# Optimization experiments

Hardware: AMD Instinct MI355X
Metric: run time of the kernel (lower is better)

Reference implementation:

```python
import jax, jax.numpy as jnp
import numpy as np

B, S, C = 4, 2048, 1024
E, H = 1024, 16
D = E // H  # head_dim = 64


def setup_inputs() -> dict:
    key = jax.random.key(0)
    k1, k2, k3, k4, k5 = jax.random.split(key, 5)
    s = 1.0 / np.sqrt(C)
    return {
        "x": jax.random.normal(k1, (B, S, C), dtype=jnp.float32),
        "w_qkv": jax.random.uniform(k2, (C, 3 * E), minval=-s, maxval=s, dtype=jnp.float32),
        "b_qkv": jax.random.uniform(k3, (3 * E,), minval=-s, maxval=s, dtype=jnp.float32),
        "w_out": jax.random.uniform(k4, (E, E), minval=-1.0 / np.sqrt(E), maxval=1.0 / np.sqrt(E), dtype=jnp.float32),
        "b_out": jax.random.uniform(k5, (E,), minval=-1.0 / np.sqrt(E), maxval=1.0 / np.sqrt(E), dtype=jnp.float32),
    }


def reference(x, w_qkv, b_qkv, w_out, b_out):
    b, s, _ = x.shape
    qkv = x @ w_qkv + b_qkv                      # [B,S,3E]
    qkv = qkv.reshape(b, s, 3, H, D)
    q = qkv[:, :, 0].transpose(0, 2, 1, 3)       # [B,H,S,D]
    k = qkv[:, :, 1].transpose(0, 2, 1, 3)
    v = qkv[:, :, 2].transpose(0, 2, 1, 3)
    scale = jnp.asarray(D, x.dtype) ** 0.5
    scores = jnp.einsum("bhqd,bhkd->bhqk", q, k) / scale
    attn = jax.nn.softmax(scores, axis=-1)       # dropout is identity in eval mode
    out = jnp.einsum("bhqk,bhkd->bhqd", attn, v)
    out = out.transpose(0, 2, 1, 3).reshape(b, s, E)
    return out @ w_out + b_out
```

## Files before the change

### kernel.cpp

```cpp
#include <hip/hip_runtime.h>


typedef _Float16 f16;
typedef f16 f16x2 __attribute__((ext_vector_type(2)));
typedef f16 f16x4 __attribute__((ext_vector_type(4)));
typedef f16 f16x8 __attribute__((ext_vector_type(8)));
typedef float f32x4 __attribute__((ext_vector_type(4)));

typedef const __attribute__((address_space(1))) void* gas_ptr;
typedef __attribute__((address_space(3))) void* lds_ptr;

__device__ __forceinline__ void load_lds16(const void* g, void* s) {
  __builtin_amdgcn_global_load_lds((gas_ptr)g, (lds_ptr)s, 16, 0, 0);
}

__device__ __forceinline__ f32x4 mfma16(f16x8 a, f16x8 b, f32x4 c) {
  return __builtin_amdgcn_mfma_f32_16x16x32_f16(a, b, c, 0, 0, 0);
}

__device__ __forceinline__ f16x2 pk2(float a, float b) {
  return __builtin_bit_cast(f16x2, __builtin_amdgcn_cvt_pkrtz(a, b));
}

__global__ __launch_bounds__(256) void cvt_x(const float* __restrict__ in, f16* __restrict__ out) {
  int i = blockIdx.x * 256 + threadIdx.x;
  const float4* p = (const float4*)in;
  float4 a = p[2 * i], b = p[2 * i + 1];
  f16x8 o;
  o[0] = (f16)a.x; o[1] = (f16)a.y; o[2] = (f16)a.z; o[3] = (f16)a.w;
  o[4] = (f16)b.x; o[5] = (f16)b.y; o[6] = (f16)b.z; o[7] = (f16)b.w;
  *(f16x8*)(out + 8 * (long)i) = o;
}

__global__ __launch_bounds__(256) void tconv(const float* __restrict__ in, f16* __restrict__ out,
                                             int R, int C) {
  __shared__ float t[32][33];
  int c0 = blockIdx.x * 32, r0 = blockIdx.y * 32;
  int tx = threadIdx.x, ty = threadIdx.y;
#pragma unroll
  for (int j = 0; j < 4; ++j)
    t[ty + 8 * j][tx] = in[(long)(r0 + ty + 8 * j) * C + c0 + tx];
  __syncthreads();
#pragma unroll
  for (int j = 0; j < 4; ++j)
    out[(long)(c0 + ty + 8 * j) * R + r0 + tx] = (f16)t[tx][ty + 8 * j];
}

__global__ __launch_bounds__(256) void qkv_gemm(const f16* __restrict__ A, const f16* __restrict__ BT,
                                                const float* __restrict__ bias,
                                                f16* __restrict__ Qs, f16* __restrict__ Kk,
                                                f16* __restrict__ Vt) {
  __shared__ __align__(16) f16 lA[2][128 * 64];
  __shared__ __align__(16) f16 lB[2][128 * 64];
  const int K = 1024;
  int tid = threadIdx.x, w = tid >> 6, lane = tid & 63, l16 = lane & 15, quad = lane >> 4;
  int wm = (w >> 1) * 64, wn = (w & 1) * 64;
  int id = blockIdx.y * gridDim.x + blockIdx.x;
  int xcd = id & 7, cch = id >> 3;
  int bx = xcd * 8 + (cch & 7), by = cch >> 3;
  int blockM = bx * 128, blockN = by * 128;
  int sw = l16 & 7;
  f32x4 acc[4][4] = {};

  auto stage = [&](int kt) {
    int k0 = kt * 64;
    f16* dA = lA[kt & 1];
    f16* dB = lB[kt & 1];
#pragma unroll
    for (int i = 0; i < 4; ++i) {
      int c = i * 256 + tid;
      int row = c >> 3;
      int sc = (c & 7) ^ (row & 7);
      load_lds16(A + (long)(blockM + row) * K + k0 + sc * 8, dA + c * 8);
      load_lds16(BT + (long)(blockN + row) * K + k0 + sc * 8, dB + c * 8);
    }
  };

  stage(0);
  asm volatile("s_waitcnt vmcnt(0)" ::: "memory");
  __builtin_amdgcn_s_barrier();

  for (int t = 0; t < 16; ++t) {
    if (t < 15) stage(t + 1);
    const f16* cA = lA[t & 1];
    const f16* cB = lB[t & 1];
#pragma unroll
    for (int ks = 0; ks < 2; ++ks) {
      f16x8 af[4], bf[4];
#pragma unroll
      for (int mb = 0; mb < 4; ++mb)
        af[mb] = *(const f16x8*)&cA[(wm + mb * 16 + l16) * 64 + ((ks * 4 + quad) ^ sw) * 8];
#pragma unroll
      for (int nb = 0; nb < 4; ++nb)
        bf[nb] = *(const f16x8*)&cB[(wn + nb * 16 + l16) * 64 + ((ks * 4 + quad) ^ sw) * 8];
      __builtin_amdgcn_s_setprio(1);
#pragma unroll
      for (int mb = 0; mb < 4; ++mb)
#pragma unroll
        for (int nb = 0; nb < 4; ++nb)
          acc[mb][nb] = mfma16(af[mb], bf[nb], acc[mb][nb]);
      __builtin_amdgcn_s_setprio(0);
    }
    asm volatile("s_waitcnt vmcnt(0)" ::: "memory");
    __builtin_amdgcn_s_barrier();
  }

  int which = by >> 3;
  const float SCALE = 0.18033688011112042f;
#pragma unroll
  for (int nb = 0; nb < 4; ++nb) {
    int col = blockN + wn + nb * 16 + l16;
    int hd = col & 1023, h = hd >> 6, d = hd & 63;
    float bv = bias[col];
#pragma unroll
    for (int mb = 0; mb < 4; ++mb) {
      int row0 = blockM + wm + mb * 16 + quad * 4;
      int b = row0 >> 11, s0 = row0 & 2047;
      if (which == 2) {
        f16x2 a = pk2(acc[mb][nb][0] + bv, acc[mb][nb][1] + bv);
        f16x2 c = pk2(acc[mb][nb][2] + bv, acc[mb][nb][3] + bv);
        *(f16x4*)&Vt[((b * 16 + h) * 64 + d) * 2048 + s0] =
            __builtin_shufflevector(a, c, 0, 1, 2, 3);
      } else if (which == 0) {
#pragma unroll
        for (int r = 0; r < 4; ++r)
          Qs[((b * 16 + h) * 2048 + s0 + r) * 64 + d] = (f16)((acc[mb][nb][r] + bv) * SCALE);
      } else {
#pragma unroll
        for (int r = 0; r < 4; ++r)
          Kk[((b * 16 + h) * 2048 + s0 + r) * 64 + d] = (f16)(acc[mb][nb][r] + bv);
      }
    }
  }
}

__global__ __launch_bounds__(512, 4) void attn(const f16* __restrict__ Qs, const f16* __restrict__ Kk,
                                               const f16* __restrict__ Vt, f16* __restrict__ ctx) {
  __shared__ __align__(16) f16 lK[2][64 * 72];
  __shared__ __align__(16) f16 lV[2][64 * 72];
  int id = blockIdx.y * gridDim.x + blockIdx.x;
  int swz = (id & 7) * 64 + (id >> 3);
  int qt = swz & 7, bh = swz >> 3;
  int tid = threadIdx.x, lane = tid & 63, l16 = lane & 15, quad = lane >> 4;
  int w = tid >> 6;
  const f16* Qbase = Qs + ((long)bh * 2048 + qt * 256 + w * 32) * 64;
  const f16* Kbh = Kk + (long)bh * 2048 * 64;
  const f16* Vbh = Vt + (long)bh * 64 * 2048;

  f16x8 qf[2][2];
#pragma unroll
  for (int rb = 0; rb < 2; ++rb)
#pragma unroll
    for (int ks = 0; ks < 2; ++ks)
      qf[rb][ks] = *(const f16x8*)(Qbase + (rb * 16 + l16) * 64 + ks * 32 + quad * 8);

  f32x4 of[2][4] = {};
  f32x4 osum[2] = {};
  const f16 one = (f16)1.f;
  const f16x8 vone8 = {one, one, one, one, one, one, one, one};

  int rs = tid >> 3, o = (tid & 7) * 8;
  int koff = o & 31;
  int cperm = (o & 32) + ((koff & 12) << 1) + ((koff >> 4) << 2);

  {
    *(float4*)&lK[0][rs * 72 + o] = *(const float4*)(Kbh + rs * 64 + o);
    float4 pv = *(const float4*)(Vbh + (long)rs * 2048 + o);
    f16x8 v8 = __builtin_bit_cast(f16x8, pv);
    *(f16x4*)&lV[0][rs * 72 + cperm] = __builtin_shufflevector(v8, v8, 0, 1, 2, 3);
    *(f16x4*)&lV[0][rs * 72 + cperm + 8] = __builtin_shufflevector(v8, v8, 4, 5, 6, 7);
  }
  __syncthreads();

  for (int kt = 0; kt < 32; ++kt) {
    int cur = kt & 1, nxt = cur ^ 1;

    float4 pk0, pv0;
    if (kt < 31) {
      int kb0 = (kt + 1) * 64;
      pk0 = *(const float4*)(Kbh + (kb0 + rs) * 64 + o);
      pv0 = *(const float4*)(Vbh + (long)rs * 2048 + kb0 + o);
    }

    __builtin_amdgcn_s_setprio(1);
#pragma unroll
    for (int kp = 0; kp < 2; ++kp) {
      f16x4 pah[2][2];
#pragma unroll
      for (int kbh = 0; kbh < 2; ++kbh) {
        int kb = kp * 2 + kbh;
        f16x8 kf0 = *(const f16x8*)&lK[cur][(kb * 16 + l16) * 72 + quad * 8];
        f16x8 kf1 = *(const f16x8*)&lK[cur][(kb * 16 + l16) * 72 + 32 + quad * 8];
#pragma unroll
        for (int rb = 0; rb < 2; ++rb) {
          f32x4 z = {};
          z = mfma16(kf0, qf[rb][0], z);
          z = mfma16(kf1, qf[rb][1], z);
          float p0 = __builtin_amdgcn_exp2f(z[0]);
          float p1 = __builtin_amdgcn_exp2f(z[1]);
          float p2 = __builtin_amdgcn_exp2f(z[2]);
          float p3 = __builtin_amdgcn_exp2f(z[3]);
          pah[rb][kbh] = __builtin_shufflevector(pk2(p0, p1), pk2(p2, p3), 0, 1, 2, 3);
        }
      }
      f16x8 pa[2];
      pa[0] = __builtin_shufflevector(pah[0][0], pah[0][1], 0, 1, 2, 3, 4, 5, 6, 7);
      pa[1] = __builtin_shufflevector(pah[1][0], pah[1][1], 0, 1, 2, 3, 4, 5, 6, 7);

#pragma unroll
      for (int db = 0; db < 4; ++db) {
        f16x8 vf = *(const f16x8*)&lV[cur][(db * 16 + l16) * 72 + kp * 32 + quad * 8];
#pragma unroll
        for (int rb = 0; rb < 2; ++rb)
          of[rb][db] = mfma16(pa[rb], vf, of[rb][db]);
      }
#pragma unroll
      for (int rb = 0; rb < 2; ++rb)
        osum[rb] = mfma16(pa[rb], vone8, osum[rb]);
    }
    __builtin_amdgcn_s_setprio(0);

    if (kt < 31) {
      *(float4*)&lK[nxt][rs * 72 + o] = pk0;
      f16x8 v8 = __builtin_bit_cast(f16x8, pv0);
      *(f16x4*)&lV[nxt][rs * 72 + cperm] = __builtin_shufflevector(v8, v8, 0, 1, 2, 3);
      *(f16x4*)&lV[nxt][rs * 72 + cperm + 8] = __builtin_shufflevector(v8, v8, 4, 5, 6, 7);
      __syncthreads();
    }
  }

  int b = bh >> 4, h = bh & 15;
  long token0 = (long)b * 2048 + qt * 256 + w * 32;
#pragma unroll
  for (int rb = 0; rb < 2; ++rb) {
    float inv[4];
#pragma unroll
    for (int r = 0; r < 4; ++r) inv[r] = 1.0f / osum[rb][r];
#pragma unroll
    for (int db = 0; db < 4; ++db)
#pragma unroll
      for (int r = 0; r < 4; ++r)
        ctx[(token0 + rb * 16 + quad * 4 + r) * 1024 + h * 64 + db * 16 + l16] =
            (f16)(of[rb][db][r] * inv[r]);
  }
}

__global__ __launch_bounds__(256) void proj_gemm(const f16* __restrict__ A, const f16* __restrict__ BT,
                                                 const float* __restrict__ bias,
                                                 float* __restrict__ out) {
  __shared__ __align__(16) f16 lA[2][128 * 64];
  __shared__ __align__(16) f16 lB[2][128 * 64];
  const int K = 1024;
  int tid = threadIdx.x, w = tid >> 6, lane = tid & 63, l16 = lane & 15, quad = lane >> 4;
  int wm = (w >> 1) * 64, wn = (w & 1) * 64;
  int id = blockIdx.y * gridDim.x + blockIdx.x;
  int xcd = id & 7, cch = id >> 3;
  int bx = xcd * 8 + (cch & 7), by = cch >> 3;
  int blockM = bx * 128, blockN = by * 128;
  int sw = l16 & 7;
  f32x4 acc[4][4] = {};

  auto stage = [&](int kt) {
    int k0 = kt * 64;
    f16* dA = lA[kt & 1];
    f16* dB = lB[kt & 1];
#pragma unroll
    for (int i = 0; i < 4; ++i) {
      int c = i * 256 + tid;
      int row = c >> 3;
      int sc = (c & 7) ^ (row & 7);
      load_lds16(A + (long)(blockM + row) * K + k0 + sc * 8, dA + c * 8);
      load_lds16(BT + (long)(blockN + row) * K + k0 + sc * 8, dB + c * 8);
    }
  };

  stage(0);
  asm volatile("s_waitcnt vmcnt(0)" ::: "memory");
  __builtin_amdgcn_s_barrier();

  for (int t = 0; t < 16; ++t) {
    if (t < 15) stage(t + 1);
    const f16* cA = lA[t & 1];
    const f16* cB = lB[t & 1];
#pragma unroll
    for (int ks = 0; ks < 2; ++ks) {
      f16x8 af[4], bf[4];
#pragma unroll
      for (int mb = 0; mb < 4; ++mb)
        af[mb] = *(const f16x8*)&cA[(wm + mb * 16 + l16) * 64 + ((ks * 4 + quad) ^ sw) * 8];
#pragma unroll
      for (int nb = 0; nb < 4; ++nb)
        bf[nb] = *(const f16x8*)&cB[(wn + nb * 16 + l16) * 64 + ((ks * 4 + quad) ^ sw) * 8];
      __builtin_amdgcn_s_setprio(1);
#pragma unroll
      for (int mb = 0; mb < 4; ++mb)
#pragma unroll
        for (int nb = 0; nb < 4; ++nb)
          acc[mb][nb] = mfma16(af[mb], bf[nb], acc[mb][nb]);
      __builtin_amdgcn_s_setprio(0);
    }
    asm volatile("s_waitcnt vmcnt(0)" ::: "memory");
    __builtin_amdgcn_s_barrier();
  }

#pragma unroll
  for (int nb = 0; nb < 4; ++nb) {
    int col = blockN + wn + nb * 16 + l16;
    float bv = bias[col];
#pragma unroll
    for (int mb = 0; mb < 4; ++mb) {
#pragma unroll
      for (int r = 0; r < 4; ++r) {
        int row = blockM + wm + mb * 16 + quad * 4 + r;
        out[(long)row * 1024 + col] = acc[mb][nb][r] + bv;
      }
    }
  }
}

extern "C" void kernel_launch(void* const* d_in, const int* in_sizes, int n_in,
                              void* d_out, int out_size, void* d_ws, size_t ws_size,
                              hipStream_t stream) {
  const float* x     = (const float*)d_in[0];
  const float* w_qkv = (const float*)d_in[1];
  const float* b_qkv = (const float*)d_in[2];
  const float* w_out = (const float*)d_in[3];
  const float* b_out = (const float*)d_in[4];
  float* out = (float*)d_out;

  char* ws = (char*)d_ws;
  f16* xh    = (f16*)(ws);
  f16* ctx   = (f16*)(ws);
  f16* wqkvT = (f16*)(ws + 16777216);
  f16* woutT = (f16*)(ws + 23068672);
  f16* Qs    = (f16*)(ws + 25165824);
  f16* Kk    = (f16*)(ws + 41943040);
  f16* Vt    = (f16*)(ws + 58720256);

  cvt_x<<<4096, 256, 0, stream>>>(x, xh);
  tconv<<<dim3(96, 32), dim3(32, 8), 0, stream>>>(w_qkv, wqkvT, 1024, 3072);
  tconv<<<dim3(32, 32), dim3(32, 8), 0, stream>>>(w_out, woutT, 1024, 1024);
  qkv_gemm<<<dim3(64, 24), 256, 0, stream>>>(xh, wqkvT, b_qkv, Qs, Kk, Vt);
  attn<<<dim3(8, 64), 512, 0, stream>>>(Qs, Kk, Vt, ctx);
  proj_gemm<<<dim3(64, 8), 256, 0, stream>>>(ctx, woutT, b_out, out);
}
```

Before: 257.8 us.

## Fuse prep kernels, shrink attention blocks, use async K loads with XOR swizzle

Merges the x conversion and both weight transposes into one prep launch, which removes two launches. The attention kernel moves from 512 to 256 threads per block, each covering 128 query rows, so the grid doubles. K tiles are now staged through global_load_lds directly into XOR-swizzled unpadded LDS instead of passing through registers, and V uses a matching swizzle. The block-to-XCD mapping changes so each XCD handles a contiguous range of heads. Each block now reloads K/V per 128 queries rather than per 256, which doubles K/V traffic per query, and the manual vmcnt wait plus barrier adds some risk.

```diff
diff --git a/kernel.cpp b/kernel.cpp
--- a/kernel.cpp
+++ b/kernel.cpp
@@ -22,21 +22,34 @@
   return __builtin_bit_cast(f16x2, __builtin_amdgcn_cvt_pkrtz(a, b));
 }
 
-__global__ __launch_bounds__(256) void cvt_x(const float* __restrict__ in, f16* __restrict__ out) {
-  int i = blockIdx.x * 256 + threadIdx.x;
-  const float4* p = (const float4*)in;
-  float4 a = p[2 * i], b = p[2 * i + 1];
-  f16x8 o;
-  o[0] = (f16)a.x; o[1] = (f16)a.y; o[2] = (f16)a.z; o[3] = (f16)a.w;
-  o[4] = (f16)b.x; o[5] = (f16)b.y; o[6] = (f16)b.z; o[7] = (f16)b.w;
-  *(f16x8*)(out + 8 * (long)i) = o;
-}
-
-__global__ __launch_bounds__(256) void tconv(const float* __restrict__ in, f16* __restrict__ out,
-                                             int R, int C) {
+__global__ __launch_bounds__(256) void prep(const float* __restrict__ x, f16* __restrict__ xh,
+                                            const float* __restrict__ w_qkv, f16* __restrict__ wqkvT,
+                                            const float* __restrict__ w_out, f16* __restrict__ woutT) {
   __shared__ float t[32][33];
-  int c0 = blockIdx.x * 32, r0 = blockIdx.y * 32;
-  int tx = threadIdx.x, ty = threadIdx.y;
+  int bid = blockIdx.x, tid = threadIdx.x;
+  if (bid < 4096) {
+    long i = (long)bid * 256 + tid;
+    const float4* p = (const float4*)x;
+    float4 a = p[2 * i], b = p[2 * i + 1];
+    f16x8 o;
+    o[0] = (f16)a.x; o[1] = (f16)a.y; o[2] = (f16)a.z; o[3] = (f16)a.w;
+    o[4] = (f16)b.x; o[5] = (f16)b.y; o[6] = (f16)b.z; o[7] = (f16)b.w;
+    *(f16x8*)(xh + 8 * i) = o;
+    return;
+  }
+  const float* in;
+  f16* out;
+  int R, C, c0, r0;
+  if (bid < 7168) {
+    int r = bid - 4096;
+    in = w_qkv; out = wqkvT; R = 1024; C = 3072;
+    c0 = (r % 96) * 32; r0 = (r / 96) * 32;
+  } else {
+    int r = bid - 7168;
+    in = w_out; out = woutT; R = 1024; C = 1024;
+    c0 = (r & 31) * 32; r0 = (r >> 5) * 32;
+  }
+  int tx = tid & 31, ty = tid >> 5;
 #pragma unroll
   for (int j = 0; j < 4; ++j)
     t[ty + 8 * j][tx] = in[(long)(r0 + ty + 8 * j) * C + c0 + tx];
@@ -134,16 +147,17 @@
   }
 }
 
-__global__ __launch_bounds__(512, 4) void attn(const f16* __restrict__ Qs, const f16* __restrict__ Kk,
+__global__ __launch_bounds__(256, 4) void attn(const f16* __restrict__ Qs, const f16* __restrict__ Kk,
                                                const f16* __restrict__ Vt, f16* __restrict__ ctx) {
-  __shared__ __align__(16) f16 lK[2][64 * 72];
-  __shared__ __align__(16) f16 lV[2][64 * 72];
+  __shared__ __align__(16) f16 lK[2][64 * 64];
+  __shared__ __align__(16) f16 lV[2][64 * 64];
   int id = blockIdx.y * gridDim.x + blockIdx.x;
-  int swz = (id & 7) * 64 + (id >> 3);
-  int qt = swz & 7, bh = swz >> 3;
+  int xcd = id & 7, rr = id >> 3;
+  int qt = rr & 15, bh = xcd * 8 + (rr >> 4);
   int tid = threadIdx.x, lane = tid & 63, l16 = lane & 15, quad = lane >> 4;
   int w = tid >> 6;
-  const f16* Qbase = Qs + ((long)bh * 2048 + qt * 256 + w * 32) * 64;
+  int swr = l16 & 7;
+  const f16* Qbase = Qs + ((long)bh * 2048 + qt * 128 + w * 32) * 64;
   const f16* Kbh = Kk + (long)bh * 2048 * 64;
   const f16* Vbh = Vt + (long)bh * 64 * 2048;
 
@@ -159,27 +173,49 @@
   const f16 one = (f16)1.f;
   const f16x8 vone8 = {one, one, one, one, one, one, one, one};
 
-  int rs = tid >> 3, o = (tid & 7) * 8;
+  int rs = tid >> 3, o = (tid & 7) * 8, c1 = tid & 7;
+  int jj = rs & 7;
   int koff = o & 31;
-  int cperm = (o & 32) + ((koff & 12) << 1) + ((koff >> 4) << 2);
+  int Lp = (o & 32) + ((koff & 12) << 1) + ((koff >> 4) << 2);
+  int pv0b = (((Lp >> 3) ^ jj) << 4) + ((Lp & 4) << 1);
+  int pv1b = ((((Lp >> 3) + 1) ^ jj) << 4) + ((Lp & 4) << 1);
+
+  auto stageK = [&](int kt) {
+    int kb0 = kt * 64;
+    f16* dst = lK[kt & 1];
+    int r0 = rs, r1 = rs + 32;
+    load_lds16(Kbh + (kb0 + r0) * 64 + (c1 ^ (r0 & 7)) * 8, dst + tid * 8);
+    load_lds16(Kbh + (kb0 + r1) * 64 + (c1 ^ (r1 & 7)) * 8, dst + (256 + tid) * 8);
+  };
+  auto writeV = [&](int buf, float4 va, float4 vb) {
+    f16* d0 = lV[buf] + rs * 64;
+    f16* d1 = lV[buf] + (rs + 32) * 64;
+    f16x8 a8 = __builtin_bit_cast(f16x8, va);
+    f16x8 b8 = __builtin_bit_cast(f16x8, vb);
+    *(f16x4*)((char*)d0 + pv0b) = __builtin_shufflevector(a8, a8, 0, 1, 2, 3);
+    *(f16x4*)((char*)d0 + pv1b) = __builtin_shufflevector(a8, a8, 4, 5, 6, 7);
+    *(f16x4*)((char*)d1 + pv0b) = __builtin_shufflevector(b8, b8, 0, 1, 2, 3);
+    *(f16x4*)((char*)d1 + pv1b) = __builtin_shufflevector(b8, b8, 4, 5, 6, 7);
+  };
 
   {
-    *(float4*)&lK[0][rs * 72 + o] = *(const float4*)(Kbh + rs * 64 + o);
-    float4 pv = *(const float4*)(Vbh + (long)rs * 2048 + o);
-    f16x8 v8 = __builtin_bit_cast(f16x8, pv);
-    *(f16x4*)&lV[0][rs * 72 + cperm] = __builtin_shufflevector(v8, v8, 0, 1, 2, 3);
-    *(f16x4*)&lV[0][rs * 72 + cperm + 8] = __builtin_shufflevector(v8, v8, 4, 5, 6, 7);
-  }
-  __syncthreads();
+    stageK(0);
+    float4 va = *(const float4*)(Vbh + (long)rs * 2048 + o);
+    float4 vb = *(const float4*)(Vbh + (long)(rs + 32) * 2048 + o);
+    writeV(0, va, vb);
+    asm volatile("s_waitcnt vmcnt(0)" ::: "memory");
+    __builtin_amdgcn_s_barrier();
+  }
 
   for (int kt = 0; kt < 32; ++kt) {
     int cur = kt & 1, nxt = cur ^ 1;
 
-    float4 pk0, pv0;
+    float4 va, vb;
     if (kt < 31) {
       int kb0 = (kt + 1) * 64;
-      pk0 = *(const float4*)(Kbh + (kb0 + rs) * 64 + o);
-      pv0 = *(const float4*)(Vbh + (long)rs * 2048 + kb0 + o);
+      stageK(kt + 1);
+      va = *(const float4*)(Vbh + (long)rs * 2048 + kb0 + o);
+      vb = *(const float4*)(Vbh + (long)(rs + 32) * 2048 + kb0 + o);
     }
 
     __builtin_amdgcn_s_setprio(1);
@@ -189,8 +225,8 @@
 #pragma unroll
       for (int kbh = 0; kbh < 2; ++kbh) {
         int kb = kp * 2 + kbh;
-        f16x8 kf0 = *(const f16x8*)&lK[cur][(kb * 16 + l16) * 72 + quad * 8];
-        f16x8 kf1 = *(const f16x8*)&lK[cur][(kb * 16 + l16) * 72 + 32 + quad * 8];
+        f16x8 kf0 = *(const f16x8*)&lK[cur][(kb * 16 + l16) * 64 + ((quad ^ swr) << 3)];
+        f16x8 kf1 = *(const f16x8*)&lK[cur][(kb * 16 + l16) * 64 + (((4 + quad) ^ swr) << 3)];
 #pragma unroll
         for (int rb = 0; rb < 2; ++rb) {
           f32x4 z = {};
@@ -209,7 +245,7 @@
 
 #pragma unroll
       for (int db = 0; db < 4; ++db) {
-        f16x8 vf = *(const f16x8*)&lV[cur][(db * 16 + l16) * 72 + kp * 32 + quad * 8];
+        f16x8 vf = *(const f16x8*)&lV[cur][(db * 16 + l16) * 64 + (((kp * 4 + quad) ^ swr) << 3)];
 #pragma unroll
         for (int rb = 0; rb < 2; ++rb)
           of[rb][db] = mfma16(pa[rb], vf, of[rb][db]);
@@ -221,16 +257,14 @@
     __builtin_amdgcn_s_setprio(0);
 
     if (kt < 31) {
-      *(float4*)&lK[nxt][rs * 72 + o] = pk0;
-      f16x8 v8 = __builtin_bit_cast(f16x8, pv0);
-      *(f16x4*)&lV[nxt][rs * 72 + cperm] = __builtin_shufflevector(v8, v8, 0, 1, 2, 3);
-      *(f16x4*)&lV[nxt][rs * 72 + cperm + 8] = __builtin_shufflevector(v8, v8, 4, 5, 6, 7);
-      __syncthreads();
+      writeV(nxt, va, vb);
+      asm volatile("s_waitcnt vmcnt(0)" ::: "memory");
+      __builtin_amdgcn_s_barrier();
     }
   }
 
   int b = bh >> 4, h = bh & 15;
-  long token0 = (long)b * 2048 + qt * 256 + w * 32;
+  long token0 = (long)b * 2048 + qt * 128 + w * 32;
 #pragma unroll
   for (int rb = 0; rb < 2; ++rb) {
     float inv[4];
@@ -337,10 +371,8 @@
   f16* Kk    = (f16*)(ws + 41943040);
   f16* Vt    = (f16*)(ws + 58720256);
 
-  cvt_x<<<4096, 256, 0, stream>>>(x, xh);
-  tconv<<<dim3(96, 32), dim3(32, 8), 0, stream>>>(w_qkv, wqkvT, 1024, 3072);
-  tconv<<<dim3(32, 32), dim3(32, 8), 0, stream>>>(w_out, woutT, 1024, 1024);
+  prep<<<8192, 256, 0, stream>>>(x, xh, w_qkv, wqkvT, w_out, woutT);
   qkv_gemm<<<dim3(64, 24), 256, 0, stream>>>(xh, wqkvT, b_qkv, Qs, Kk, Vt);
-  attn<<<dim3(8, 64), 512, 0, stream>>>(Qs, Kk, Vt, ctx);
+  attn<<<dim3(16, 64), 256, 0, stream>>>(Qs, Kk, Vt, ctx);
   proj_gemm<<<dim3(64, 8), 256, 0, stream>>>(ctx, woutT, b_out, out);
 }
```

New measurement: 255.8 us. About the same (-0.8%).
